# Kernel optimization log

Hardware: AMD Instinct MI355X
Metric: run time of the kernel (lower is better)

The kernel has to match this reference:

```python
import jax, jax.numpy as jnp
import numpy as np

ALPHA = 0.2
NEG_INF = -9e15


def setup_inputs() -> dict:
    key = jax.random.key(0)
    k1, k2, k3, k4 = jax.random.split(key, 4)
    N, F_IN, F_OUT, H = 4096, 1, 64, 12
    x = jax.random.normal(k1, (N, F_IN), dtype=jnp.float32)
    adj = jax.random.randint(k2, (N, N), 0, 2).astype(jnp.int32)
    # per-head params stacked: W [H, F_IN, F_OUT], a [H, 2*F_OUT, 1]
    W = jax.random.normal(k3, (H, F_IN, F_OUT), dtype=jnp.float32) * 0.1
    a = jax.random.normal(k4, (H, 2 * F_OUT, 1), dtype=jnp.float32) * 0.1
    return {"x": x, "adj": adj, "W": W, "a": a}


def reference(x, adj, W, a):
    # h per head: [H, N, F_OUT]
    h = jnp.einsum('nf,hfo->hno', x, W)
    F_out = h.shape[-1]
    # a_input[i,j] = concat(h_i, h_j), so a_input @ a = h_i.a_src + h_j.a_dst
    a_src = a[:, :F_out, 0]   # [H, F_OUT]
    a_dst = a[:, F_out:, 0]   # [H, F_OUT]
    e_src = jnp.einsum('hnf,hf->hn', h, a_src)  # [H, N]
    e_dst = jnp.einsum('hnf,hf->hn', h, a_dst)  # [H, N]
    e = jax.nn.leaky_relu(e_src[:, :, None] + e_dst[:, None, :], ALPHA)  # [H,N,N]
    e = jnp.where(adj[None] > 0, e, NEG_INF)
    attn = jax.nn.softmax(e, axis=-1)           # softmax over neighbors j
    h_prime = jnp.einsum('hij,hjf->hif', attn, h)  # [H, N, F_OUT]
    # concat heads along feature dim -> [N, H*F_OUT]
    N = h_prime.shape[1]
    return jnp.transpose(h_prime, (1, 0, 2)).reshape(N, -1)
```

## Files before the change

### kernel.cpp

```cpp
#include <hip/hip_runtime.h>

#define GAT_H 12
#define GAT_N 4096
#define GAT_F 64
#define LOG2E 1.4426950408889634f


__device__ float g_tab2[GAT_H * GAT_N];
__device__ float g_sd[2 * GAT_H + 1];

__global__ __launch_bounds__(256) void gat_prep(const float* __restrict__ W,
                                                const float* __restrict__ a,
                                                const float* __restrict__ x) {
    const int b    = blockIdx.x;
    const int tid  = threadIdx.x;
    const int lane = tid & 63;
    const int wave = tid >> 6;

    if (b < GAT_H) {
        if (wave == 0) {
            const float wf = W[b * GAT_F + lane];
            float ps = wf * a[b * 2 * GAT_F + lane];
            float pd = wf * a[b * 2 * GAT_F + GAT_F + lane];
            #pragma unroll
            for (int off = 32; off > 0; off >>= 1) {
                ps += __shfl_xor(ps, off, 64);
                pd += __shfl_xor(pd, off, 64);
            }
            if (lane == 0) { g_sd[b] = ps; g_sd[GAT_H + b] = pd; }
        }
        return;
    }
    if (b == GAT_H) {
        if (wave == 0) {
            float s = 0.0f;
            #pragma unroll
            for (int j = 0; j < GAT_N / 64; ++j) s += x[j * 64 + lane];
            #pragma unroll
            for (int off = 32; off > 0; off >>= 1) s += __shfl_xor(s, off, 64);
            if (lane == 0) g_sd[2 * GAT_H] = s * (1.0f / GAT_N);
        }
        return;
    }

    const int bt    = b - (GAT_H + 1);
    const int h     = bt >> 2;
    const int chunk = bt & 3;
    const float wf  = W[h * GAT_F + lane];
    float pd = wf * a[h * 2 * GAT_F + GAT_F + lane];
    #pragma unroll
    for (int off = 32; off > 0; off >>= 1) pd += __shfl_xor(pd, off, 64);
    const float dl5 = 0.2f * pd * LOG2E;
    #pragma unroll
    for (int k = 0; k < 4; ++k) {
        const int j = chunk * 1024 + k * 256 + tid;
        g_tab2[h * GAT_N + j] = __builtin_amdgcn_exp2f(dl5 * x[j]);
    }
}

__global__ __launch_bounds__(256, 3) void gat_main(const float* __restrict__ x,
                                                   const int* __restrict__ adj,
                                                   const float* __restrict__ W,
                                                   float* __restrict__ out) {
    __shared__ float xs[GAT_N];
    __shared__ float rho_s[4][16];
    __shared__ float part[2][2][4][6][2];
    __shared__ float cbuf[4][GAT_H];

    const int tid  = threadIdx.x;
    const int row0 = blockIdx.x * 4;

    #pragma unroll
    for (int it = 0; it < GAT_N / (256 * 4); ++it)
        ((float4*)xs)[it * 256 + tid] = ((const float4*)x)[it * 256 + tid];
    if (tid < 64) {
        const int r = tid >> 4, hh = tid & 15;
        if (hh < GAT_H)
            rho_s[r][hh] =
                __builtin_amdgcn_exp2f(-0.8f * LOG2E * x[row0 + r] * g_sd[hh]);
    }
    __syncthreads();

    const int lane  = tid & 63;
    const int wave  = tid >> 6;
    const int hg    = wave >> 1;
    const int jh    = wave & 1;
    const int hbase = hg * 6;

    float rho[4][6];
    #pragma unroll
    for (int r = 0; r < 4; ++r)
        #pragma unroll
        for (int hh = 0; hh < 6; ++hh)
            rho[r][hh] = __uint_as_float(__builtin_amdgcn_readfirstlane(
                __float_as_uint(rho_s[r][hbase + hh])));

    float den[4][6], num[4][6];
    #pragma unroll
    for (int r = 0; r < 4; ++r)
        #pragma unroll
        for (int hh = 0; hh < 6; ++hh) { den[r][hh] = 0.0f; num[r][hh] = 0.0f; }

    const int4*   __restrict__ a4p = (const int4*)(adj + (size_t)row0 * GAT_N + jh * 2048);
    const float4* __restrict__ t4  = (const float4*)(g_tab2 + hbase * GAT_N + jh * 2048);
    const float4* __restrict__ x4  = (const float4*)(xs + jh * 2048);

    int4   ac[4];
    float4 xc;
    #pragma unroll
    for (int r = 0; r < 4; ++r) ac[r] = a4p[r * (GAT_N / 4) + lane];
    xc = x4[lane];

    #pragma unroll 1
    for (int it = 0; it < 8; ++it) {
        const int nxt = (it < 7 ? it + 1 : 7) * 64 + lane;
        int4 an[4];
        #pragma unroll
        for (int r = 0; r < 4; ++r) an[r] = a4p[r * (GAT_N / 4) + nxt];
        const float4 xn = x4[nxt];

        float am[4][4], axj[4][4];
        #pragma unroll
        for (int r = 0; r < 4; ++r) {
            const int* ai = (const int*)&ac[r];
            const float* xv = (const float*)&xc;
            #pragma unroll
            for (int e = 0; e < 4; ++e) {
                am[r][e]  = (float)ai[e];
                axj[r][e] = am[r][e] * xv[e];
            }
        }

        #pragma unroll
        for (int hh = 0; hh < 6; ++hh) {
            const float4 e2v = t4[hh * (GAT_N / 4) + it * 64 + lane];
            const float* e2 = (const float*)&e2v;
            float e1[4];
            #pragma unroll
            for (int e = 0; e < 4; ++e) {
                const float sq = e2[e] * e2[e];
                e1[e] = sq * sq * e2[e];
            }
            #pragma unroll
            for (int e = 0; e < 4; ++e) {
                #pragma unroll
                for (int r = 0; r < 4; ++r) {
                    const float p = fmaxf(e1[e], rho[r][hh] * e2[e]);
                    den[r][hh] = fmaf(p, am[r][e],  den[r][hh]);
                    num[r][hh] = fmaf(p, axj[r][e], num[r][hh]);
                }
            }
        }
        #pragma unroll
        for (int r = 0; r < 4; ++r) ac[r] = an[r];
        xc = xn;
    }

    #pragma unroll
    for (int r = 0; r < 4; ++r) {
        #pragma unroll
        for (int hh = 0; hh < 6; ++hh) {
            float d = den[r][hh], n = num[r][hh];
            #pragma unroll
            for (int off = 32; off > 0; off >>= 1) {
                d += __shfl_xor(d, off, 64);
                n += __shfl_xor(n, off, 64);
            }
            if (lane == 0) {
                part[jh][hg][r][hh][0] = d;
                part[jh][hg][r][hh][1] = n;
            }
        }
    }
    __syncthreads();

    if (tid < 64) {
        const int r = tid >> 4, h = tid & 15;
        if (h < GAT_H) {
            const int g  = (h >= 6) ? 1 : 0;
            const int hh = h - 6 * g;
            const float dsum = part[0][g][r][hh][0] + part[1][g][r][hh][0];
            const float nsum = part[0][g][r][hh][1] + part[1][g][r][hh][1];
            cbuf[r][h] = dsum > 0.0f ? nsum / dsum : g_sd[2 * GAT_H];
        }
    }
    __syncthreads();

    #pragma unroll
    for (int r = 0; r < 4; ++r) {
        const size_t base = (size_t)(row0 + r) * (GAT_H * GAT_F);
        #pragma unroll
        for (int k = 0; k < 3; ++k) {
            const int pos = k * 256 + tid;
            out[base + pos] = cbuf[r][pos >> 6] * W[pos];
        }
    }
}

extern "C" void kernel_launch(void* const* d_in, const int* in_sizes, int n_in,
                              void* d_out, int out_size, void* d_ws, size_t ws_size,
                              hipStream_t stream) {
    const float* x   = (const float*)d_in[0];
    const int*   adj = (const int*)d_in[1];
    const float* W   = (const float*)d_in[2];
    const float* a   = (const float*)d_in[3];
    float* out = (float*)d_out;
    (void)d_ws; (void)ws_size;

    gat_prep<<<GAT_H + 1 + 48, 256, 0, stream>>>(W, a, x);
    gat_main<<<GAT_N / 4, 256, 0, stream>>>(x, adj, W, out);
}
```

Baseline: 133.2 us.

## Split row work across 8 waves per block and drop software prefetch

The main kernel now runs 512 threads per block, with each wave handling 2 of the 4 rows instead of all 4. This halves per-thread accumulator and adjacency register state so more waves can be resident to hide memory latency. The explicit next-iteration prefetch of adjacency and x is removed. The attention weight is rewritten as max(w^4, rho)*e2, which saves one multiply per element. In exchange, every wave now loads the exp table itself, doubling table traffic per row, and the tail store loop needs a bounds guard.

```diff
diff --git a/kernel.cpp b/kernel.cpp
--- a/kernel.cpp
+++ b/kernel.cpp
@@ -58,10 +58,10 @@
     }
 }
 
-__global__ __launch_bounds__(256, 3) void gat_main(const float* __restrict__ x,
-                                                   const int* __restrict__ adj,
-                                                   const float* __restrict__ W,
-                                                   float* __restrict__ out) {
+__global__ __launch_bounds__(512) void gat_main(const float* __restrict__ x,
+                                                const int* __restrict__ adj,
+                                                const float* __restrict__ W,
+                                                float* __restrict__ out) {
     __shared__ float xs[GAT_N];
     __shared__ float rho_s[4][16];
     __shared__ float part[2][2][4][6][2];
@@ -71,8 +71,8 @@
     const int row0 = blockIdx.x * 4;
 
     #pragma unroll
-    for (int it = 0; it < GAT_N / (256 * 4); ++it)
-        ((float4*)xs)[it * 256 + tid] = ((const float4*)x)[it * 256 + tid];
+    for (int it = 0; it < GAT_N / (512 * 4); ++it)
+        ((float4*)xs)[it * 512 + tid] = ((const float4*)x)[it * 512 + tid];
     if (tid < 64) {
         const int r = tid >> 4, hh = tid & 15;
         if (hh < GAT_H)
@@ -83,81 +83,70 @@
 
     const int lane  = tid & 63;
     const int wave  = tid >> 6;
-    const int hg    = wave >> 1;
+    const int rp    = wave >> 2;
+    const int hg    = (wave >> 1) & 1;
     const int jh    = wave & 1;
     const int hbase = hg * 6;
 
-    float rho[4][6];
-    #pragma unroll
-    for (int r = 0; r < 4; ++r)
+    float rho[2][6];
+    #pragma unroll
+    for (int r = 0; r < 2; ++r)
         #pragma unroll
         for (int hh = 0; hh < 6; ++hh)
             rho[r][hh] = __uint_as_float(__builtin_amdgcn_readfirstlane(
-                __float_as_uint(rho_s[r][hbase + hh])));
-
-    float den[4][6], num[4][6];
-    #pragma unroll
-    for (int r = 0; r < 4; ++r)
+                __float_as_uint(rho_s[rp * 2 + r][hbase + hh])));
+
+    float den[2][6], num[2][6];
+    #pragma unroll
+    for (int r = 0; r < 2; ++r)
         #pragma unroll
         for (int hh = 0; hh < 6; ++hh) { den[r][hh] = 0.0f; num[r][hh] = 0.0f; }
 
-    const int4*   __restrict__ a4p = (const int4*)(adj + (size_t)row0 * GAT_N + jh * 2048);
-    const float4* __restrict__ t4  = (const float4*)(g_tab2 + hbase * GAT_N + jh * 2048);
-    const float4* __restrict__ x4  = (const float4*)(xs + jh * 2048);
-
-    int4   ac[4];
-    float4 xc;
-    #pragma unroll
-    for (int r = 0; r < 4; ++r) ac[r] = a4p[r * (GAT_N / 4) + lane];
-    xc = x4[lane];
+    const int4*   __restrict__ a4p =
+        (const int4*)(adj + (size_t)(row0 + rp * 2) * GAT_N + jh * 2048);
+    const float4* __restrict__ t4 =
+        (const float4*)(g_tab2 + hbase * GAT_N + jh * 2048);
+    const float4* __restrict__ x4 = (const float4*)(xs + jh * 2048);
 
     #pragma unroll 1
     for (int it = 0; it < 8; ++it) {
-        const int nxt = (it < 7 ? it + 1 : 7) * 64 + lane;
-        int4 an[4];
-        #pragma unroll
-        for (int r = 0; r < 4; ++r) an[r] = a4p[r * (GAT_N / 4) + nxt];
-        const float4 xn = x4[nxt];
-
-        float am[4][4], axj[4][4];
-        #pragma unroll
-        for (int r = 0; r < 4; ++r) {
-            const int* ai = (const int*)&ac[r];
-            const float* xv = (const float*)&xc;
+        const int idx = it * 64 + lane;
+        const int4   a0 = a4p[idx];
+        const int4   a1 = a4p[(GAT_N / 4) + idx];
+        const float4 xv = x4[idx];
+
+        const int*   ai0 = (const int*)&a0;
+        const int*   ai1 = (const int*)&a1;
+        const float* xp  = (const float*)&xv;
+        float am[2][4], axj[2][4];
+        #pragma unroll
+        for (int e = 0; e < 4; ++e) {
+            am[0][e]  = (float)ai0[e];
+            am[1][e]  = (float)ai1[e];
+            axj[0][e] = am[0][e] * xp[e];
+            axj[1][e] = am[1][e] * xp[e];
+        }
+
+        #pragma unroll
+        for (int hh = 0; hh < 6; ++hh) {
+            const float4 e2v = t4[hh * (GAT_N / 4) + idx];
+            const float* e2  = (const float*)&e2v;
             #pragma unroll
             for (int e = 0; e < 4; ++e) {
-                am[r][e]  = (float)ai[e];
-                axj[r][e] = am[r][e] * xv[e];
-            }
-        }
-
-        #pragma unroll
-        for (int hh = 0; hh < 6; ++hh) {
-            const float4 e2v = t4[hh * (GAT_N / 4) + it * 64 + lane];
-            const float* e2 = (const float*)&e2v;
-            float e1[4];
-            #pragma unroll
-            for (int e = 0; e < 4; ++e) {
-                const float sq = e2[e] * e2[e];
-                e1[e] = sq * sq * e2[e];
-            }
-            #pragma unroll
-            for (int e = 0; e < 4; ++e) {
+                const float w  = e2[e] * e2[e];
+                const float w4 = w * w;
                 #pragma unroll
-                for (int r = 0; r < 4; ++r) {
-                    const float p = fmaxf(e1[e], rho[r][hh] * e2[e]);
+                for (int r = 0; r < 2; ++r) {
+                    const float p = fmaxf(w4, rho[r][hh]) * e2[e];
                     den[r][hh] = fmaf(p, am[r][e],  den[r][hh]);
                     num[r][hh] = fmaf(p, axj[r][e], num[r][hh]);
                 }
             }
         }
-        #pragma unroll
-        for (int r = 0; r < 4; ++r) ac[r] = an[r];
-        xc = xn;
-    }
-
-    #pragma unroll
-    for (int r = 0; r < 4; ++r) {
+    }
+
+    #pragma unroll
+    for (int r = 0; r < 2; ++r) {
         #pragma unroll
         for (int hh = 0; hh < 6; ++hh) {
             float d = den[r][hh], n = num[r][hh];
@@ -167,8 +156,8 @@
                 n += __shfl_xor(n, off, 64);
             }
             if (lane == 0) {
-                part[jh][hg][r][hh][0] = d;
-                part[jh][hg][r][hh][1] = n;
+                part[jh][hg][rp * 2 + r][hh][0] = d;
+                part[jh][hg][rp * 2 + r][hh][1] = n;
             }
         }
     }
@@ -190,9 +179,10 @@
     for (int r = 0; r < 4; ++r) {
         const size_t base = (size_t)(row0 + r) * (GAT_H * GAT_F);
         #pragma unroll
-        for (int k = 0; k < 3; ++k) {
-            const int pos = k * 256 + tid;
-            out[base + pos] = cbuf[r][pos >> 6] * W[pos];
+        for (int k = 0; k < 2; ++k) {
+            const int pos = k * 512 + tid;
+            if (pos < GAT_H * GAT_F)
+                out[base + pos] = cbuf[r][pos >> 6] * W[pos];
         }
     }
 }
@@ -208,5 +198,5 @@
     (void)d_ws; (void)ws_size;
 
     gat_prep<<<GAT_H + 1 + 48, 256, 0, stream>>>(W, a, x);
-    gat_main<<<GAT_N / 4, 256, 0, stream>>>(x, adj, W, out);
+    gat_main<<<GAT_N / 4, 512, 0, stream>>>(x, adj, W, out);
 }
```

New measurement: 143.2 us. 7.5% more time.
